# Kernel optimization log

Hardware: AMD Instinct MI355X
Metric: run time of the kernel (lower is better)

Reference implementation:

```python
import jax, jax.numpy as jnp
import numpy as np

N, F, P, H, D = 8, 64, 25, 6, 192
HD = D // H
T = F * P
MAX_HOP = 5  # hop values in [0, MAX_HOP)
SCALE = HD ** -0.5


def _mlp(pos, w1, b1, w2, b2):
    # Linear(1, mlp_dim) -> ReLU -> Linear(mlp_dim, num_heads)
    return jax.nn.relu(pos @ w1.T + b1) @ w2.T + b2


def setup_inputs() -> dict:
    key = jax.random.key(0)
    ks = jax.random.split(key, 16)
    inp = {
        'x': jax.random.normal(ks[0], (N, T, D), jnp.float32),
        'qkv_w': jax.random.normal(ks[1], (3 * D, D), jnp.float32) * (D ** -0.5),
        'proj_w': jax.random.normal(ks[2], (D, D), jnp.float32) * (D ** -0.5),
        'proj_b': jax.random.normal(ks[3], (D,), jnp.float32) * 0.01,
        't_w1': jax.random.normal(ks[4], (D, 1), jnp.float32),
        't_b1': jax.random.normal(ks[5], (D,), jnp.float32) * 0.01,
        't_w2': jax.random.normal(ks[6], (H, D), jnp.float32) * (D ** -0.5),
        't_b2': jax.random.normal(ks[7], (H,), jnp.float32) * 0.01,
        'h_w1': jax.random.normal(ks[8], (D, 1), jnp.float32),
        'h_b1': jax.random.normal(ks[9], (D,), jnp.float32) * 0.01,
        'h_w2': jax.random.normal(ks[10], (H, D), jnp.float32) * (D ** -0.5),
        'h_b2': jax.random.normal(ks[11], (H,), jnp.float32) * 0.01,
        'outer': jax.random.uniform(ks[12], (H, P, P), jnp.float32),
        'alpha': jax.random.uniform(ks[13], (1,), jnp.float32),
        'hops': jax.random.randint(ks[14], (P, P), 0, MAX_HOP, jnp.int32),
    }
    # row-normalize outer like A / A.sum(-1, keepdims=True)
    inp['outer'] = inp['outer'] / inp['outer'].sum(-1, keepdims=True)
    return inp


def reference(x, qkv_w, proj_w, proj_b, t_w1, t_b1, t_w2, t_b2,
              h_w1, h_b1, h_w2, h_b2, outer, alpha, hops):
    qkv = (x @ qkv_w.T).reshape(N, T, 3, H, HD).transpose(2, 0, 3, 1, 4)
    q, k, v = qkv[0], qkv[1], qkv[2]

    # raw scores
    attn = jnp.einsum('nhtc,nhsc->nhts', q, k)

    # temporal dynamic RPB: table over 2F-1 relative frame offsets
    coords_t = jnp.arange(-(F - 1), F, dtype=jnp.float32)[:, None]  # (2F-1,1)
    table_t = _mlp(coords_t, t_w1, t_b1, t_w2, t_b2)                # (2F-1,H)
    rel_idx = jnp.arange(F)[:, None] - jnp.arange(F)[None, :] + (F - 1)
    bias_f = table_t[rel_idx].transpose(2, 0, 1)                    # (H,F,F)
    bias_temporal = jnp.repeat(jnp.repeat(bias_f, P, axis=1), P, axis=2)  # (H,T,T)

    # hop RPB: table over hop distances, tiled over frames
    coords_h = jnp.arange(MAX_HOP, dtype=jnp.float32)[:, None]      # (MAX_HOP,1)
    table_h = _mlp(coords_h, h_w1, h_b1, h_w2, h_b2)                # (MAX_HOP,H)
    bias_p = table_h[hops].transpose(2, 0, 1)                       # (H,P,P)
    bias_hop = jnp.tile(bias_p, (1, F, F))                          # (H,T,T)

    attn = jax.nn.softmax((attn + bias_hop + bias_temporal) * SCALE, axis=-1)

    # relational term: block-diag(outer) applied per frame, fused without
    # materializing the (H,T,T) block-diagonal matrix
    out = alpha[0] * jnp.einsum('nhts,nhsc->nhtc', attn, v)
    v_r = v.reshape(N, H, F, P, HD)
    out = out + jnp.einsum('hpq,nhfqd->nhfpd', outer, v_r).reshape(N, H, T, HD)

    out = out.transpose(0, 2, 1, 3).reshape(N, T, D)
    return out @ proj_w.T + proj_b
```

## Files before the change

kernel.cpp:

```cpp
#include <hip/hip_runtime.h>
#include <math.h>

#define N_ 8
#define F_ 64
#define P_ 25
#define H_ 6
#define D_ 192
#define HD_ 32
#define T_ 1600
#define SC2F 0.25503486f

typedef short bf16x8 __attribute__((ext_vector_type(8)));
typedef float f32x4 __attribute__((ext_vector_type(4)));
typedef unsigned int uint4v __attribute__((ext_vector_type(4)));

__device__ __forceinline__ unsigned short f2bf(float f) {
    unsigned int u = __float_as_uint(f);
    u += 0x7fffu + ((u >> 16) & 1u);
    return (unsigned short)(u >> 16);
}
__device__ __forceinline__ float bf2f(unsigned short s) {
    return __uint_as_float(((unsigned int)s) << 16);
}
__device__ __forceinline__ unsigned int pack2bf(float lo, float hi) {
    return (unsigned int)f2bf(lo) | ((unsigned int)f2bf(hi) << 16);
}
__device__ __forceinline__ unsigned int cvt_pk_bf16(float lo, float hi) {
    unsigned int r;
    asm("v_cvt_pk_bf16_f32 %0, %1, %2" : "=v"(r) : "v"(lo), "v"(hi));
    return r;
}

__global__ __launch_bounds__(256) void prep_kernel(
    const float* __restrict__ t_w1, const float* __restrict__ t_b1,
    const float* __restrict__ t_w2, const float* __restrict__ t_b2,
    const float* __restrict__ h_w1, const float* __restrict__ h_b1,
    const float* __restrict__ h_w2, const float* __restrict__ h_b2,
    float* __restrict__ tt, float* __restrict__ th,
    unsigned int* __restrict__ augA)
{
    int b = blockIdx.x;
    if (b >= 132) {
        int tau = b - 132;
        int sb = threadIdx.x >> 6, lane = threadIdx.x & 63;
        int g = lane >> 4, qi = lane & 15;
        int s = tau * 64 + sb * 16 + qi;
        int fs = (s * 5243) >> 17;
        int ps = s - fs * 25;
        int fs0 = ((tau * 64) * 5243) >> 17;
        int dfs = fs - fs0;
        unsigned int a[4];
        #pragma unroll
        for (int jj = 0; jj < 4; ++jj) {
            int k0 = g * 8 + 2 * jj, k1 = k0 + 1;
            bool c0 = (k0 < 4) ? (dfs == k0) : (ps == k0 - 4);
            bool c1 = (k1 < 4) ? (dfs == k1) : (ps == k1 - 4);
            a[jj] = (c0 ? 0x3F80u : 0u) | (c1 ? 0x3F800000u : 0u);
        }
        uint4v w = {a[0], a[1], a[2], a[3]};
        *(uint4v*)&augA[((size_t)(tau * 4 + sb) * 64 + lane) * 4] = w;
        return;
    }
    __shared__ float hid[192];
    bool is_t = (b < 127);
    float pos = is_t ? (float)(b - 63) : (float)(b - 127);
    const float* w1 = is_t ? t_w1 : h_w1;
    const float* b1 = is_t ? t_b1 : h_b1;
    const float* w2 = is_t ? t_w2 : h_w2;
    const float* b2 = is_t ? t_b2 : h_b2;
    int t = threadIdx.x;
    if (t < 192) hid[t] = fmaxf(pos * w1[t] + b1[t], 0.0f);
    __syncthreads();
    if (t < 6) {
        float s = b2[t];
        for (int j = 0; j < 192; ++j) s += w2[t * 192 + j] * hid[j];
        s *= SC2F;
        if (is_t) tt[t * 127 + b] = s;
        else      th[t * 5 + (b - 127)] = s;
    }
}

__global__ __launch_bounds__(256) void qkv_gemm_kernel(
    const float* __restrict__ x, const float* __restrict__ w,
    unsigned short* __restrict__ qout, unsigned short* __restrict__ kout,
    unsigned short* __restrict__ vout)
{
    __shared__ __align__(16) unsigned short alds[64][200];
    __shared__ __align__(16) unsigned short blds[64][72];

    int b = blockIdx.x;
    int bm = b % 200, bn = b / 200;
    int row0 = bm * 64, col0 = bn * 64;
    int tid = threadIdx.x, lane = tid & 63, wv = tid >> 6;
    int g = lane >> 4, qi = lane & 15;

    #pragma unroll
    for (int p = 0; p < 12; ++p) {
        int fid = tid + p * 256;
        int r = fid / 48, c4 = (fid % 48) * 4;
        float4 a4 = *(const float4*)&x[(size_t)(row0 + r) * 192 + c4];
        uint2 pk;
        pk.x = pack2bf(a4.x, a4.y);
        pk.y = pack2bf(a4.z, a4.w);
        *(uint2*)&alds[r][c4] = pk;
    }

    f32x4 acc[4];
    #pragma unroll
    for (int nt = 0; nt < 4; ++nt) acc[nt] = (f32x4){0.f, 0.f, 0.f, 0.f};

    for (int k0 = 0; k0 < 192; k0 += 64) {
        __syncthreads();
        #pragma unroll
        for (int p = 0; p < 4; ++p) {
            int fid = tid + p * 256;
            int j = fid >> 4, k4 = (fid & 15) * 4;
            float4 w4 = *(const float4*)&w[(size_t)(col0 + j) * 192 + k0 + k4];
            uint2 pk;
            pk.x = pack2bf(w4.x, w4.y);
            pk.y = pack2bf(w4.z, w4.w);
            *(uint2*)&blds[j][k4] = pk;
        }
        __syncthreads();
        #pragma unroll
        for (int ks = 0; ks < 2; ++ks) {
            bf16x8 af = *(const bf16x8*)&alds[wv * 16 + qi][k0 + ks * 32 + g * 8];
            #pragma unroll
            for (int nt = 0; nt < 4; ++nt) {
                bf16x8 bf = *(const bf16x8*)&blds[nt * 16 + qi][ks * 32 + g * 8];
                acc[nt] = __builtin_amdgcn_mfma_f32_16x16x32_bf16(af, bf, acc[nt], 0, 0, 0);
            }
        }
    }

    #pragma unroll
    for (int nt = 0; nt < 4; ++nt) {
        int col = col0 + nt * 16 + qi;
        int three = col / 192;
        int rem = col - three * 192;
        int h = rem >> 5, c = rem & 31;
        unsigned short* dst = (three == 0) ? qout : ((three == 1) ? kout : vout);
        float scl = (three == 0) ? SC2F : 1.0f;
        #pragma unroll
        for (int r = 0; r < 4; ++r) {
            int row = row0 + wv * 16 + 4 * g + r;
            int n = row / 1600, t = row - n * 1600;
            dst[((size_t)(n * 6 + h) * 1600 + t) * 32 + c] = f2bf(acc[nt][r] * scl);
        }
    }
}

__global__ __launch_bounds__(256) void attn_kernel(
    const unsigned short* __restrict__ qw, const unsigned short* __restrict__ kw,
    const unsigned short* __restrict__ vw, const float* __restrict__ tt,
    const float* __restrict__ th, const int* __restrict__ hops,
    const unsigned int* __restrict__ augA,
    const float* __restrict__ alpha_p, float* __restrict__ aout)
{
    __shared__ __align__(16) unsigned short ks[2][64][40];
    __shared__ __align__(16) unsigned int vts32[2][32][34];
    __shared__ __align__(16) unsigned int plds[4][16][36];
    __shared__ unsigned int tthi[127], ttlo[127];

    int b = blockIdx.x;
    int serial = (b & 7) * 150 + (b >> 3);
    int nh = serial / 25;
    int qt = serial % 25;
    int h = nh % 6;
    int t0 = qt * 64;

    int tid = threadIdx.x;
    int lane = tid & 63, wv = tid >> 6;
    int g = lane >> 4, qi = lane & 15;
    int i = tid & 127;
    bool isK = (wv < 2);

    const unsigned short* qb = qw + (size_t)nh * 51200;
    const unsigned short* kb = kw + (size_t)nh * 51200;
    const unsigned short* vb = vw + (size_t)nh * 51200;
    float* ab = aout + (size_t)nh * 51200;

    if (tid < 127) {
        float a = tt[h * 127 + tid];
        float bm1 = tt[h * 127 + max(tid - 1, 0)];
        unsigned short ha = f2bf(a), hb = f2bf(bm1);
        tthi[tid] = (unsigned)ha | ((unsigned)hb << 16);
        ttlo[tid] = (unsigned)f2bf(a - bf2f(ha)) |
                    ((unsigned)f2bf(bm1 - bf2f(hb)) << 16);
    }

    int tq = t0 + wv * 16 + qi;
    int ft = (tq * 5243) >> 17;
    int pt = tq - ft * 25;

    bf16x8 qfrag = *(const bf16x8*)&qb[(size_t)tq * 32 + g * 8];

    unsigned int baug_hi[4], baug_lo[4];
    #pragma unroll
    for (int jj = 0; jj < 4; ++jj) {
        int k0 = g * 8 + 2 * jj, k1 = k0 + 1;
        float v0 = 0.f, v1 = 0.f;
        if (k0 >= 4 && k0 < 29) v0 = th[h * 5 + hops[pt * 25 + (k0 - 4)]];
        if (k1 >= 4 && k1 < 29) v1 = th[h * 5 + hops[pt * 25 + (k1 - 4)]];
        unsigned short h0 = f2bf(v0), h1 = f2bf(v1);
        unsigned short l0 = f2bf(v0 - bf2f(h0)), l1 = f2bf(v1 - bf2f(h1));
        baug_hi[jj] = (unsigned)h0 | ((unsigned)h1 << 16);
        baug_lo[jj] = (unsigned)l0 | ((unsigned)l1 << 16);
    }

    float l = 0.f;
    f32x4 O0 = {0.f, 0.f, 0.f, 0.f}, O1 = {0.f, 0.f, 0.f, 0.f};

    const uint4v* augp = (const uint4v*)augA;

    if (isK) {
        int row = i >> 1, c16 = (i & 1) * 16;
        const unsigned short* src = kb + (size_t)row * 32 + c16;
        uint4 a = *(const uint4*)src;
        uint4 bq = *(const uint4*)(src + 8);
        *(uint4*)&ks[0][row][c16] = a;
        *(uint4*)&ks[0][row][c16 + 8] = bq;
    } else {
        int p = i >> 2, c8v = (i & 3) * 8;
        const unsigned short* src = vb + (size_t)(2 * p) * 32 + c8v;
        union { uint4 u; unsigned short s[8]; } a, bq;
        a.u = *(const uint4*)src;
        bq.u = *(const uint4*)(src + 32);
        #pragma unroll
        for (int j = 0; j < 8; ++j)
            vts32[0][c8v + j][p] = (unsigned)a.s[j] | ((unsigned)bq.s[j] << 16);
    }
    uint4v augr[4];
    #pragma unroll
    for (int sb = 0; sb < 4; ++sb) augr[sb] = augp[(size_t)sb * 64 + lane];
    __syncthreads();

    for (int tau = 0; tau < 25; ++tau) {
        int cur = tau & 1, nxt = cur ^ 1;
        int s0 = tau * 64;
        bool more = (tau < 24);

        uint4 r0 = {0, 0, 0, 0}, r1 = {0, 0, 0, 0};
        uint4v augn[4];
        if (more) {
            if (isK) {
                int row = i >> 1, c16 = (i & 1) * 16;
                const unsigned short* src = kb + (size_t)(s0 + 64 + row) * 32 + c16;
                r0 = *(const uint4*)src;
                r1 = *(const uint4*)(src + 8);
            } else {
                int p = i >> 2, c8v = (i & 3) * 8;
                const unsigned short* src = vb + (size_t)(s0 + 64 + 2 * p) * 32 + c8v;
                r0 = *(const uint4*)src;
                r1 = *(const uint4*)(src + 32);
            }
            #pragma unroll
            for (int sb = 0; sb < 4; ++sb)
                augn[sb] = augp[(size_t)((tau + 1) * 4 + sb) * 64 + lane];
        }

        int fs0 = (s0 * 5243) >> 17;

        unsigned int bh0 = baug_hi[0], bh1 = baug_hi[1];
        unsigned int bl0 = baug_lo[0], bl1 = baug_lo[1];
        if (g == 0) {
            int base = ft - fs0 + 63;
            bh0 = tthi[base]; bh1 = tthi[base - 2];
            bl0 = ttlo[base]; bl1 = ttlo[base - 2];
        }
        uint4v bhiu = {bh0, bh1, baug_hi[2], baug_hi[3]};
        uint4v blou = {bl0, bl1, baug_lo[2], baug_lo[3]};
        bf16x8 bhif = __builtin_bit_cast(bf16x8, bhiu);
        bf16x8 blof = __builtin_bit_cast(bf16x8, blou);

        f32x4 sfr[4];
        #pragma unroll
        for (int sb = 0; sb < 4; ++sb) {
            bf16x8 af = __builtin_bit_cast(bf16x8, augr[sb]);
            bf16x8 kf = *(const bf16x8*)&ks[cur][sb * 16 + qi][g * 8];
            f32x4 cz = {0.f, 0.f, 0.f, 0.f};
            f32x4 cb = __builtin_amdgcn_mfma_f32_16x16x32_bf16(af, blof, cz, 0, 0, 0);
            cb = __builtin_amdgcn_mfma_f32_16x16x32_bf16(af, bhif, cb, 0, 0, 0);
            sfr[sb] = __builtin_amdgcn_mfma_f32_16x16x32_bf16(kf, qfrag, cb, 0, 0, 0);
        }

        #pragma unroll
        for (int sb = 0; sb < 4; ++sb) {
            float p0 = __builtin_exp2f(sfr[sb][0]);
            float p1 = __builtin_exp2f(sfr[sb][1]);
            float p2 = __builtin_exp2f(sfr[sb][2]);
            float p3 = __builtin_exp2f(sfr[sb][3]);
            l += (p0 + p1) + (p2 + p3);
            uint2 wp;
            wp.x = cvt_pk_bf16(p0, p1);
            wp.y = cvt_pk_bf16(p2, p3);
            *(uint2*)&plds[wv][qi][sb * 8 + 2 * g] = wp;
        }

        if (more) {
            if (isK) {
                int row = i >> 1, c16 = (i & 1) * 16;
                *(uint4*)&ks[nxt][row][c16] = r0;
                *(uint4*)&ks[nxt][row][c16 + 8] = r1;
            } else {
                int p = i >> 2, c8v = (i & 3) * 8;
                union { uint4 u; unsigned short s[8]; } a, bq;
                a.u = r0; bq.u = r1;
                #pragma unroll
                for (int j = 0; j < 8; ++j)
                    vts32[nxt][c8v + j][p] = (unsigned)a.s[j] | ((unsigned)bq.s[j] << 16);
            }
            #pragma unroll
            for (int sb = 0; sb < 4; ++sb) augr[sb] = augn[sb];
        }

        #pragma unroll
        for (int c = 0; c < 2; ++c) {
            bf16x8 paf = *(const bf16x8*)&plds[wv][qi][c * 16 + 4 * g];
            uint2 la = *(const uint2*)&vts32[cur][qi][c * 16 + 4 * g];
            uint2 lb = *(const uint2*)&vts32[cur][qi][c * 16 + 4 * g + 2];
            uint2 ha = *(const uint2*)&vts32[cur][16 + qi][c * 16 + 4 * g];
            uint2 hb = *(const uint2*)&vts32[cur][16 + qi][c * 16 + 4 * g + 2];
            uint4v u0 = {la.x, la.y, lb.x, lb.y};
            uint4v u1 = {ha.x, ha.y, hb.x, hb.y};
            bf16x8 v0f = __builtin_bit_cast(bf16x8, u0);
            bf16x8 v1f = __builtin_bit_cast(bf16x8, u1);
            O0 = __builtin_amdgcn_mfma_f32_16x16x32_bf16(paf, v0f, O0, 0, 0, 0);
            O1 = __builtin_amdgcn_mfma_f32_16x16x32_bf16(paf, v1f, O1, 0, 0, 0);
        }

        __syncthreads();
    }

    l += __shfl_xor(l, 16, 64);
    l += __shfl_xor(l, 32, 64);
    float alpha = alpha_p[0];
    float winv = alpha / l;
    int trow = t0 + wv * 16;
    #pragma unroll
    for (int r = 0; r < 4; ++r) {
        float wr = __uint_as_float(
            __builtin_amdgcn_ds_bpermute((4 * g + r) << 2, __float_as_uint(winv)));
        ab[(size_t)(trow + 4 * g + r) * 32 + qi] = O0[r] * wr;
        ab[(size_t)(trow + 4 * g + r) * 32 + 16 + qi] = O1[r] * wr;
    }
}

__global__ __launch_bounds__(256) void rel_kernel(
    const float* __restrict__ ab, const unsigned short* __restrict__ vw,
    const float* __restrict__ outer, unsigned short* __restrict__ comb)
{
    __shared__ float olds[25][26];
    __shared__ unsigned short vlds[25][32];
    int b = blockIdx.x;
    int n = b / 384;
    int h = (b / 64) % 6;
    int f = b & 63;
    int tid = threadIdx.x;

    for (int e = tid; e < 625; e += 256) olds[e / 25][e % 25] = outer[h * 625 + e];
    size_t vbase = ((size_t)(n * 6 + h) * 1600 + f * 25) * 32;
    for (int e = tid; e < 400; e += 256)
        ((unsigned int*)&vlds[0][0])[e] = *(const unsigned int*)&vw[vbase + e * 2];
    __syncthreads();

    size_t abase = vbase;
    size_t cbase = ((size_t)n * 1600 + f * 25) * 192 + h * 32;
    for (int e = tid; e < 800; e += 256) {
        int p = e >> 5, c = e & 31;
        float s = ab[abase + e];
        #pragma unroll
        for (int q = 0; q < 25; ++q) s += olds[p][q] * bf2f(vlds[q][c]);
        comb[cbase + (size_t)p * 192 + c] = f2bf(s);
    }
}

__global__ __launch_bounds__(256) void proj_gemm_kernel(
    const unsigned short* __restrict__ comb, const float* __restrict__ pw,
    const float* __restrict__ pb, float* __restrict__ out)
{
    __shared__ __align__(16) unsigned short alds[64][200];
    __shared__ __align__(16) unsigned short blds[64][72];

    int b = blockIdx.x;
    int bm = b % 200, bn = b / 200;
    int row0 = bm * 64, col0 = bn * 64;
    int tid = threadIdx.x, lane = tid & 63, wv = tid >> 6;
    int g = lane >> 4, qi = lane & 15;

    #pragma unroll
    for (int p = 0; p < 6; ++p) {
        int fid = tid + p * 256;
        int r = fid / 24, c8 = (fid % 24) * 8;
        *(uint4*)&alds[r][c8] = *(const uint4*)&comb[(size_t)(row0 + r) * 192 + c8];
    }

    f32x4 acc[4];
    #pragma unroll
    for (int nt = 0; nt < 4; ++nt) acc[nt] = (f32x4){0.f, 0.f, 0.f, 0.f};

    for (int k0 = 0; k0 < 192; k0 += 64) {
        __syncthreads();
        #pragma unroll
        for (int p = 0; p < 4; ++p) {
            int fid = tid + p * 256;
            int j = fid >> 4, k4 = (fid & 15) * 4;
            float4 w4 = *(const float4*)&pw[(size_t)(col0 + j) * 192 + k0 + k4];
            uint2 pk;
            pk.x = pack2bf(w4.x, w4.y);
            pk.y = pack2bf(w4.z, w4.w);
            *(uint2*)&blds[j][k4] = pk;
        }
        __syncthreads();
        #pragma unroll
        for (int ks = 0; ks < 2; ++ks) {
            bf16x8 af = *(const bf16x8*)&alds[wv * 16 + qi][k0 + ks * 32 + g * 8];
            #pragma unroll
            for (int nt = 0; nt < 4; ++nt) {
                bf16x8 bf = *(const bf16x8*)&blds[nt * 16 + qi][ks * 32 + g * 8];
                acc[nt] = __builtin_amdgcn_mfma_f32_16x16x32_bf16(af, bf, acc[nt], 0, 0, 0);
            }
        }
    }

    #pragma unroll
    for (int nt = 0; nt < 4; ++nt) {
        int col = col0 + nt * 16 + qi;
        float bias = pb[col];
        #pragma unroll
        for (int r = 0; r < 4; ++r) {
            int row = row0 + wv * 16 + 4 * g + r;
            out[(size_t)row * 192 + col] = acc[nt][r] + bias;
        }
    }
}

extern "C" void kernel_launch(void* const* d_in, const int* in_sizes, int n_in,
                              void* d_out, int out_size, void* d_ws, size_t ws_size,
                              hipStream_t stream)
{
    const float* x      = (const float*)d_in[0];
    const float* qkv_w  = (const float*)d_in[1];
    const float* proj_w = (const float*)d_in[2];
    const float* proj_b = (const float*)d_in[3];
    const float* t_w1   = (const float*)d_in[4];
    const float* t_b1   = (const float*)d_in[5];
    const float* t_w2   = (const float*)d_in[6];
    const float* t_b2   = (const float*)d_in[7];
    const float* h_w1   = (const float*)d_in[8];
    const float* h_b1   = (const float*)d_in[9];
    const float* h_w2   = (const float*)d_in[10];
    const float* h_b2   = (const float*)d_in[11];
    const float* outer  = (const float*)d_in[12];
    const float* alpha  = (const float*)d_in[13];
    const int*   hops   = (const int*)d_in[14];
    float* out = (float*)d_out;

    char* w8 = (char*)d_ws;
    float* tt = (float*)w8;
    float* th = (float*)(w8 + 3072);
    unsigned int* augA = (unsigned int*)(w8 + 10240);
    unsigned short* qb = (unsigned short*)(w8 + 112640);
    unsigned short* kb = qb + 2457600;
    unsigned short* vb = kb + 2457600;
    float* ab = (float*)(w8 + 112640 + 3 * 4915200);
    unsigned short* comb = qb;

    prep_kernel<<<157, 256, 0, stream>>>(t_w1, t_b1, t_w2, t_b2,
                                         h_w1, h_b1, h_w2, h_b2, tt, th, augA);
    qkv_gemm_kernel<<<1800, 256, 0, stream>>>(x, qkv_w, qb, kb, vb);
    attn_kernel<<<1200, 256, 0, stream>>>(qb, kb, vb, tt, th, hops, augA,
                                          alpha, ab);
    rel_kernel<<<3072, 256, 0, stream>>>(ab, vb, outer, comb);
    proj_gemm_kernel<<<600, 256, 0, stream>>>(comb, proj_w, proj_b, out);
}
```

Baseline: 103.0 us.

## Double attention query tile to 128 rows with 512-thread blocks

The attention kernel now processes 128 query rows per block using 8 waves, sharing each staged K/V tile across twice as many queries. The K/V loading work is split across the 4 K-waves and 4 V-waves with narrower per-thread loads. This reduces redundant global K/V loads and the number of blocks. The tail tile is padded: out-of-range queries are clamped and their stores masked, which wastes some compute on the last tile and may reduce occupancy.

```diff
diff --git a/kernel.cpp b/kernel.cpp
--- a/kernel.cpp
+++ b/kernel.cpp
@@ -150,7 +150,7 @@
     }
 }
 
-__global__ __launch_bounds__(256) void attn_kernel(
+__global__ __launch_bounds__(512) void attn_kernel(
     const unsigned short* __restrict__ qw, const unsigned short* __restrict__ kw,
     const unsigned short* __restrict__ vw, const float* __restrict__ tt,
     const float* __restrict__ th, const int* __restrict__ hops,
@@ -159,21 +159,20 @@
 {
     __shared__ __align__(16) unsigned short ks[2][64][40];
     __shared__ __align__(16) unsigned int vts32[2][32][34];
-    __shared__ __align__(16) unsigned int plds[4][16][36];
+    __shared__ __align__(16) unsigned int plds[8][16][36];
     __shared__ unsigned int tthi[127], ttlo[127];
 
     int b = blockIdx.x;
-    int serial = (b & 7) * 150 + (b >> 3);
-    int nh = serial / 25;
-    int qt = serial % 25;
+    int serial = (b & 7) * 78 + (b >> 3);
+    int nh = serial / 13;
+    int qt2 = serial - nh * 13;
     int h = nh % 6;
-    int t0 = qt * 64;
+    int t0 = qt2 * 128;
 
     int tid = threadIdx.x;
     int lane = tid & 63, wv = tid >> 6;
     int g = lane >> 4, qi = lane & 15;
-    int i = tid & 127;
-    bool isK = (wv < 2);
+    bool isK = (wv < 4);
 
     const unsigned short* qb = qw + (size_t)nh * 51200;
     const unsigned short* kb = kw + (size_t)nh * 51200;
@@ -189,11 +188,13 @@
                     ((unsigned)f2bf(bm1 - bf2f(hb)) << 16);
     }
 
-    int tq = t0 + wv * 16 + qi;
-    int ft = (tq * 5243) >> 17;
-    int pt = tq - ft * 25;
-
-    bf16x8 qfrag = *(const bf16x8*)&qb[(size_t)tq * 32 + g * 8];
+    int tq = t0 + (wv >> 2) * 64 + (wv & 3) * 16 + qi;
+    bool valid = (tq < 1600);
+    int tqc = min(tq, 1599);
+    int ft = (tqc * 5243) >> 17;
+    int pt = tqc - ft * 25;
+
+    bf16x8 qfrag = *(const bf16x8*)&qb[(size_t)tqc * 32 + g * 8];
 
     unsigned int baug_hi[4], baug_lo[4];
     #pragma unroll
@@ -213,22 +214,18 @@
 
     const uint4v* augp = (const uint4v*)augA;
 
+    int krow = (tid & 255) >> 2, kc8 = (tid & 3) * 8;
+    int vi = tid - 256, vp = vi >> 3, vc4 = (vi & 7) * 4;
+
     if (isK) {
-        int row = i >> 1, c16 = (i & 1) * 16;
-        const unsigned short* src = kb + (size_t)row * 32 + c16;
-        uint4 a = *(const uint4*)src;
-        uint4 bq = *(const uint4*)(src + 8);
-        *(uint4*)&ks[0][row][c16] = a;
-        *(uint4*)&ks[0][row][c16 + 8] = bq;
+        *(uint4*)&ks[0][krow][kc8] = *(const uint4*)&kb[(size_t)krow * 32 + kc8];
     } else {
-        int p = i >> 2, c8v = (i & 3) * 8;
-        const unsigned short* src = vb + (size_t)(2 * p) * 32 + c8v;
-        union { uint4 u; unsigned short s[8]; } a, bq;
-        a.u = *(const uint4*)src;
-        bq.u = *(const uint4*)(src + 32);
-        #pragma unroll
-        for (int j = 0; j < 8; ++j)
-            vts32[0][c8v + j][p] = (unsigned)a.s[j] | ((unsigned)bq.s[j] << 16);
+        union { uint2 u; unsigned short s[4]; } a, c;
+        a.u = *(const uint2*)&vb[(size_t)(2 * vp) * 32 + vc4];
+        c.u = *(const uint2*)&vb[(size_t)(2 * vp + 1) * 32 + vc4];
+        #pragma unroll
+        for (int j = 0; j < 4; ++j)
+            vts32[0][vc4 + j][vp] = (unsigned)a.s[j] | ((unsigned)c.s[j] << 16);
     }
     uint4v augr[4];
     #pragma unroll
@@ -240,19 +237,15 @@
         int s0 = tau * 64;
         bool more = (tau < 24);
 
-        uint4 r0 = {0, 0, 0, 0}, r1 = {0, 0, 0, 0};
+        uint4 kr = {0, 0, 0, 0};
+        uint2 va = {0, 0}, vc = {0, 0};
         uint4v augn[4];
         if (more) {
             if (isK) {
-                int row = i >> 1, c16 = (i & 1) * 16;
-                const unsigned short* src = kb + (size_t)(s0 + 64 + row) * 32 + c16;
-                r0 = *(const uint4*)src;
-                r1 = *(const uint4*)(src + 8);
+                kr = *(const uint4*)&kb[(size_t)(s0 + 64 + krow) * 32 + kc8];
             } else {
-                int p = i >> 2, c8v = (i & 3) * 8;
-                const unsigned short* src = vb + (size_t)(s0 + 64 + 2 * p) * 32 + c8v;
-                r0 = *(const uint4*)src;
-                r1 = *(const uint4*)(src + 32);
+                va = *(const uint2*)&vb[(size_t)(s0 + 64 + 2 * vp) * 32 + vc4];
+                vc = *(const uint2*)&vb[(size_t)(s0 + 64 + 2 * vp + 1) * 32 + vc4];
             }
             #pragma unroll
             for (int sb = 0; sb < 4; ++sb)
@@ -299,16 +292,13 @@
 
         if (more) {
             if (isK) {
-                int row = i >> 1, c16 = (i & 1) * 16;
-                *(uint4*)&ks[nxt][row][c16] = r0;
-                *(uint4*)&ks[nxt][row][c16 + 8] = r1;
+                *(uint4*)&ks[nxt][krow][kc8] = kr;
             } else {
-                int p = i >> 2, c8v = (i & 3) * 8;
-                union { uint4 u; unsigned short s[8]; } a, bq;
-                a.u = r0; bq.u = r1;
+                union { uint2 u; unsigned short s[4]; } a, c;
+                a.u = va; c.u = vc;
                 #pragma unroll
-                for (int j = 0; j < 8; ++j)
-                    vts32[nxt][c8v + j][p] = (unsigned)a.s[j] | ((unsigned)bq.s[j] << 16);
+                for (int j = 0; j < 4; ++j)
+                    vts32[nxt][vc4 + j][vp] = (unsigned)a.s[j] | ((unsigned)c.s[j] << 16);
             }
             #pragma unroll
             for (int sb = 0; sb < 4; ++sb) augr[sb] = augn[sb];
@@ -336,13 +326,15 @@
     l += __shfl_xor(l, 32, 64);
     float alpha = alpha_p[0];
     float winv = alpha / l;
-    int trow = t0 + wv * 16;
+    int trow = t0 + (wv >> 2) * 64 + (wv & 3) * 16;
     #pragma unroll
     for (int r = 0; r < 4; ++r) {
         float wr = __uint_as_float(
             __builtin_amdgcn_ds_bpermute((4 * g + r) << 2, __float_as_uint(winv)));
-        ab[(size_t)(trow + 4 * g + r) * 32 + qi] = O0[r] * wr;
-        ab[(size_t)(trow + 4 * g + r) * 32 + 16 + qi] = O1[r] * wr;
+        if (valid) {
+            ab[(size_t)(trow + 4 * g + r) * 32 + qi] = O0[r] * wr;
+            ab[(size_t)(trow + 4 * g + r) * 32 + 16 + qi] = O1[r] * wr;
+        }
     }
 }
 
@@ -469,8 +461,8 @@
     prep_kernel<<<157, 256, 0, stream>>>(t_w1, t_b1, t_w2, t_b2,
                                          h_w1, h_b1, h_w2, h_b2, tt, th, augA);
     qkv_gemm_kernel<<<1800, 256, 0, stream>>>(x, qkv_w, qb, kb, vb);
-    attn_kernel<<<1200, 256, 0, stream>>>(qb, kb, vb, tt, th, hops, augA,
-                                          alpha, ab);
+    attn_kernel<<<624, 512, 0, stream>>>(qb, kb, vb, tt, th, hops, augA,
+                                         alpha, ab);
     rel_kernel<<<3072, 256, 0, stream>>>(ab, vb, outer, comb);
     proj_gemm_kernel<<<600, 256, 0, stream>>>(comb, proj_w, proj_b, out);
 }
```

Measured after the change: 113.1 us. 9.8% more time.

## Fuse relational outer-term into attention epilogue and drop rel_kernel

Applied to the files above, without the earlier changes.

The attention kernel's epilogue now stages the per-head outer matrix and the V rows for the frames covered by its 64-row query tile into the reused K shared-memory buffer. It adds the block-diagonal relational term in registers and writes the combined bf16 result straight to the projection input buffer. This removes a separate kernel launch and the fp32 attention-output round trip through global memory. In exchange, each attention block does an extra shared-memory load phase, a sync and a 25-term dot product per output in its tail. The combined output also moves to its own workspace region instead of aliasing the Q buffer.

```diff
diff --git a/kernel.cpp b/kernel.cpp
--- a/kernel.cpp
+++ b/kernel.cpp
@@ -154,8 +154,8 @@
     const unsigned short* __restrict__ qw, const unsigned short* __restrict__ kw,
     const unsigned short* __restrict__ vw, const float* __restrict__ tt,
     const float* __restrict__ th, const int* __restrict__ hops,
-    const unsigned int* __restrict__ augA,
-    const float* __restrict__ alpha_p, float* __restrict__ aout)
+    const unsigned int* __restrict__ augA, const float* __restrict__ outer,
+    const float* __restrict__ alpha_p, unsigned short* __restrict__ comb)
 {
     __shared__ __align__(16) unsigned short ks[2][64][40];
     __shared__ __align__(16) unsigned int vts32[2][32][34];
@@ -167,6 +167,7 @@
     int nh = serial / 25;
     int qt = serial % 25;
     int h = nh % 6;
+    int n = nh / 6;
     int t0 = qt * 64;
 
     int tid = threadIdx.x;
@@ -178,7 +179,6 @@
     const unsigned short* qb = qw + (size_t)nh * 51200;
     const unsigned short* kb = kw + (size_t)nh * 51200;
     const unsigned short* vb = vw + (size_t)nh * 51200;
-    float* ab = aout + (size_t)nh * 51200;
 
     if (tid < 127) {
         float a = tt[h * 127 + tid];
@@ -304,11 +304,11 @@
                 *(uint4*)&ks[nxt][row][c16 + 8] = r1;
             } else {
                 int p = i >> 2, c8v = (i & 3) * 8;
-                union { uint4 u; unsigned short s[8]; } a, bq;
-                a.u = r0; bq.u = r1;
+                union { uint4 u; unsigned short s[8]; } a, c;
+                a.u = r0; c.u = r1;
                 #pragma unroll
                 for (int j = 0; j < 8; ++j)
-                    vts32[nxt][c8v + j][p] = (unsigned)a.s[j] | ((unsigned)bq.s[j] << 16);
+                    vts32[nxt][c8v + j][p] = (unsigned)a.s[j] | ((unsigned)c.s[j] << 16);
             }
             #pragma unroll
             for (int sb = 0; sb < 4; ++sb) augr[sb] = augn[sb];
@@ -332,6 +332,21 @@
         __syncthreads();
     }
 
+    float* olds = (float*)&ks[0][0][0];
+    unsigned short* vl = (unsigned short*)((char*)&ks[0][0][0] + 2720);
+    unsigned int* vl32 = (unsigned int*)vl;
+    const unsigned int* vb32 = (const unsigned int*)vb;
+    int f_lo = (t0 * 5243) >> 17;
+
+    for (int e = tid; e < 625; e += 256)
+        olds[(e / 25) * 26 + (e % 25)] = outer[h * 625 + e];
+    for (int w = tid; w < 1600; w += 256) {
+        int row = w >> 4, c2 = w & 15;
+        int grow = min(f_lo * 25 + row, 1599);
+        vl32[row * 16 + c2] = vb32[(size_t)grow * 16 + c2];
+    }
+    __syncthreads();
+
     l += __shfl_xor(l, 16, 64);
     l += __shfl_xor(l, 32, 64);
     float alpha = alpha_p[0];
@@ -341,37 +356,20 @@
     for (int r = 0; r < 4; ++r) {
         float wr = __uint_as_float(
             __builtin_amdgcn_ds_bpermute((4 * g + r) << 2, __float_as_uint(winv)));
-        ab[(size_t)(trow + 4 * g + r) * 32 + qi] = O0[r] * wr;
-        ab[(size_t)(trow + 4 * g + r) * 32 + 16 + qi] = O1[r] * wr;
-    }
-}
-
-__global__ __launch_bounds__(256) void rel_kernel(
-    const float* __restrict__ ab, const unsigned short* __restrict__ vw,
-    const float* __restrict__ outer, unsigned short* __restrict__ comb)
-{
-    __shared__ float olds[25][26];
-    __shared__ unsigned short vlds[25][32];
-    int b = blockIdx.x;
-    int n = b / 384;
-    int h = (b / 64) % 6;
-    int f = b & 63;
-    int tid = threadIdx.x;
-
-    for (int e = tid; e < 625; e += 256) olds[e / 25][e % 25] = outer[h * 625 + e];
-    size_t vbase = ((size_t)(n * 6 + h) * 1600 + f * 25) * 32;
-    for (int e = tid; e < 400; e += 256)
-        ((unsigned int*)&vlds[0][0])[e] = *(const unsigned int*)&vw[vbase + e * 2];
-    __syncthreads();
-
-    size_t abase = vbase;
-    size_t cbase = ((size_t)n * 1600 + f * 25) * 192 + h * 32;
-    for (int e = tid; e < 800; e += 256) {
-        int p = e >> 5, c = e & 31;
-        float s = ab[abase + e];
-        #pragma unroll
-        for (int q = 0; q < 25; ++q) s += olds[p][q] * bf2f(vlds[q][c]);
-        comb[cbase + (size_t)p * 192 + c] = f2bf(s);
+        int t = trow + 4 * g + r;
+        int ftt = (t * 5243) >> 17;
+        int ptt = t - ftt * 25;
+        int vbr = (ftt - f_lo) * 25;
+        float rel0 = 0.f, rel1 = 0.f;
+        #pragma unroll
+        for (int q = 0; q < 25; ++q) {
+            float ow = olds[ptt * 26 + q];
+            rel0 += ow * bf2f(vl[(vbr + q) * 32 + qi]);
+            rel1 += ow * bf2f(vl[(vbr + q) * 32 + 16 + qi]);
+        }
+        size_t cb = ((size_t)(n * 1600 + t)) * 192 + h * 32;
+        comb[cb + qi] = f2bf(O0[r] * wr + rel0);
+        comb[cb + 16 + qi] = f2bf(O1[r] * wr + rel1);
     }
 }
 
@@ -463,14 +461,12 @@
     unsigned short* qb = (unsigned short*)(w8 + 112640);
     unsigned short* kb = qb + 2457600;
     unsigned short* vb = kb + 2457600;
-    float* ab = (float*)(w8 + 112640 + 3 * 4915200);
-    unsigned short* comb = qb;
+    unsigned short* comb = (unsigned short*)(w8 + 112640 + 3 * 4915200);
 
     prep_kernel<<<157, 256, 0, stream>>>(t_w1, t_b1, t_w2, t_b2,
                                          h_w1, h_b1, h_w2, h_b2, tt, th, augA);
     qkv_gemm_kernel<<<1800, 256, 0, stream>>>(x, qkv_w, qb, kb, vb);
     attn_kernel<<<1200, 256, 0, stream>>>(qb, kb, vb, tt, th, hops, augA,
-                                          alpha, ab);
-    rel_kernel<<<3072, 256, 0, stream>>>(ab, vb, outer, comb);
+                                          outer, alpha, comb);
     proj_gemm_kernel<<<600, 256, 0, stream>>>(comb, proj_w, proj_b, out);
 }
```

Result: faster. 99.01 us (-3.9%).
